# Performance work log

Measured on AMD Instinct MI355X. Metric: run time of the kernel, lower is better.

## Reference

```python
import jax, jax.numpy as jnp
import numpy as np

N = 12288
IN_DIM = 128
OUT_DIM = 128
LR_SLOPE = 0.01
NEG_INF = -9e16


def setup_inputs() -> dict:
    key = jax.random.key(0)
    k1, k2, k3, k4 = jax.random.split(key, 4)
    emb_mat = jax.random.normal(k1, (N, IN_DIM), dtype=jnp.float32)
    adj_mat = jax.random.randint(k2, (N, N), 0, 2, dtype=jnp.int32)
    # xavier-normal-ish init for params
    W = jax.random.normal(k3, (OUT_DIM, IN_DIM), dtype=jnp.float32) * (2.0 / (IN_DIM + OUT_DIM)) ** 0.5
    a = jax.random.normal(k4, (2 * OUT_DIM, 1), dtype=jnp.float32) * (2.0 / (2 * OUT_DIM + 1)) ** 0.5
    return {"emb_mat": emb_mat, "adj_mat": adj_mat, "W": W, "a": a}


def reference(emb_mat, adj_mat, W, a):
    out_dim = W.shape[0]
    e_new = emb_mat @ W.T                       # [N, D_out]
    a1 = a[:out_dim, :]                         # [D_out, 1]
    a2 = a[out_dim:, :]                         # [D_out, 1]
    source_scores = e_new @ a1                  # [N, 1]
    target_scores = e_new @ a2                  # [N, 1]
    e = source_scores + target_scores.T         # [N, N] outer sum
    e = jax.nn.leaky_relu(e, negative_slope=LR_SLOPE)
    e = jnp.where(adj_mat > 0, e, NEG_INF)
    attention = jax.nn.softmax(e, axis=-1)      # [N, N]
    e_transf = attention @ e_new                # [N, D_out]
    return jax.nn.relu(e_transf)
```

## Files before the change

kernel.cpp:

```cpp
#include <hip/hip_runtime.h>


#define NN 12288
#define DIM 128
#define CSPLIT 4
#define COLS_PER (NN / CSPLIT)

typedef __bf16 bf16x8 __attribute__((ext_vector_type(8)));
typedef float f32x4 __attribute__((ext_vector_type(4)));

__global__ __launch_bounds__(256) void k1_gemm(const float* __restrict__ emb,
                                               const float* __restrict__ W,
                                               const float* __restrict__ a,
                                               __bf16* __restrict__ Vt,
                                               float* __restrict__ s,
                                               float* __restrict__ t) {
  const int lane = threadIdx.x & 63;
  const int wave = threadIdx.x >> 6;
  const int m = lane & 15;
  const int quad = lane >> 4;
  const int row0 = blockIdx.x * 128 + wave * 32;

  f32x4 acc[2][8];
#pragma unroll
  for (int mt = 0; mt < 2; mt++)
#pragma unroll
    for (int nb = 0; nb < 8; nb++) acc[mt][nb] = (f32x4){0.f, 0.f, 0.f, 0.f};

#pragma unroll
  for (int ks = 0; ks < 4; ks++) {
    const int k0 = ks * 32 + quad * 8;
    bf16x8 af[2];
#pragma unroll
    for (int mt = 0; mt < 2; mt++) {
      const float* ep = emb + (size_t)(row0 + mt * 16 + m) * DIM + k0;
      float4 lo = *(const float4*)ep;
      float4 hi = *(const float4*)(ep + 4);
      af[mt] = (bf16x8){(__bf16)lo.x, (__bf16)lo.y, (__bf16)lo.z, (__bf16)lo.w,
                        (__bf16)hi.x, (__bf16)hi.y, (__bf16)hi.z, (__bf16)hi.w};
    }
#pragma unroll
    for (int nb = 0; nb < 8; nb++) {
      const float* wp = W + (size_t)(nb * 16 + m) * DIM + k0;
      float4 lo = *(const float4*)wp;
      float4 hi = *(const float4*)(wp + 4);
      bf16x8 bf = {(__bf16)lo.x, (__bf16)lo.y, (__bf16)lo.z, (__bf16)lo.w,
                   (__bf16)hi.x, (__bf16)hi.y, (__bf16)hi.z, (__bf16)hi.w};
      acc[0][nb] = __builtin_amdgcn_mfma_f32_16x16x32_bf16(af[0], bf, acc[0][nb], 0, 0, 0);
      acc[1][nb] = __builtin_amdgcn_mfma_f32_16x16x32_bf16(af[1], bf, acc[1][nb], 0, 0, 0);
    }
  }

  float a1v[8], a2v[8];
#pragma unroll
  for (int nb = 0; nb < 8; nb++) {
    a1v[nb] = a[nb * 16 + m];
    a2v[nb] = a[DIM + nb * 16 + m];
  }
#pragma unroll
  for (int mt = 0; mt < 2; mt++) {
#pragma unroll
    for (int r = 0; r < 4; r++) {
      const int gr = row0 + mt * 16 + quad * 4 + r;
      float ps = 0.f, pt = 0.f;
#pragma unroll
      for (int nb = 0; nb < 8; nb++) {
        float e = acc[mt][nb][r];
        ps += e * a1v[nb];
        pt += e * a2v[nb];
        Vt[(size_t)(nb * 16 + m) * NN + gr] = (__bf16)e;
      }
      ps += __shfl_xor(ps, 1); ps += __shfl_xor(ps, 2);
      ps += __shfl_xor(ps, 4); ps += __shfl_xor(ps, 8);
      pt += __shfl_xor(pt, 1); pt += __shfl_xor(pt, 2);
      pt += __shfl_xor(pt, 4); pt += __shfl_xor(pt, 8);
      if (m == 0) { s[gr] = ps; t[gr] = pt; }
    }
  }
}

__global__ __launch_bounds__(256) void ktmax(const float* __restrict__ t,
                                             float* __restrict__ tmax) {
  __shared__ float red[256];
  float mx = -1e30f;
  for (int i = threadIdx.x; i < NN; i += 256) mx = fmaxf(mx, t[i]);
  red[threadIdx.x] = mx;
  __syncthreads();
  for (int off = 128; off; off >>= 1) {
    if ((int)threadIdx.x < off) red[threadIdx.x] = fmaxf(red[threadIdx.x], red[threadIdx.x + off]);
    __syncthreads();
  }
  if (threadIdx.x == 0) *tmax = red[0];
}

__global__ __launch_bounds__(256) void k2_attn(const int* __restrict__ adj,
                                               const __bf16* __restrict__ Vt,
                                               const float* __restrict__ s,
                                               const float* __restrict__ t,
                                               const float* __restrict__ tmaxp,
                                               float* __restrict__ out,
                                               float* __restrict__ lws) {
  const int lane = threadIdx.x & 63;
  const int wave = threadIdx.x >> 6;
  const int m = lane & 15;
  const int quad = lane >> 4;
  const int row0 = blockIdx.x * 128 + wave * 32;
  const int col0 = blockIdx.y * COLS_PER;
  const int rowA = row0 + m;
  const int rowB = rowA + 16;

  const float Tmax = *tmaxp;
  const float sA = s[rowA], sB = s[rowB];
  const float uA = sA + Tmax, uB = sB + Tmax;
  const float mA = fmaxf(uA, 0.01f * uA);
  const float mB = fmaxf(uB, 0.01f * uB);

  const int* adjA = adj + (size_t)rowA * NN + col0 + quad * 8;
  const int* adjB = adj + (size_t)rowB * NN + col0 + quad * 8;
  const float* tp = t + col0 + quad * 8;
  const __bf16* vp = Vt + (size_t)m * NN + col0 + quad * 8;

  f32x4 accA[8], accB[8];
#pragma unroll
  for (int nb = 0; nb < 8; nb++) {
    accA[nb] = (f32x4){0.f, 0.f, 0.f, 0.f};
    accB[nb] = (f32x4){0.f, 0.f, 0.f, 0.f};
  }
  float lA = 0.f, lB = 0.f;

  for (int kb = 0; kb < COLS_PER; kb += 32) {
    int4 aA0 = *(const int4*)(adjA + kb);
    int4 aA1 = *(const int4*)(adjA + kb + 4);
    int4 aB0 = *(const int4*)(adjB + kb);
    int4 aB1 = *(const int4*)(adjB + kb + 4);
    float4 t0 = *(const float4*)(tp + kb);
    float4 t1 = *(const float4*)(tp + kb + 4);
    bf16x8 bv[8];
#pragma unroll
    for (int nb = 0; nb < 8; nb++)
      bv[nb] = *(const bf16x8*)(vp + (size_t)nb * 16 * NN + kb);

    bf16x8 pA, pB;
#define PEL(frag, jj, tv, av, ss, mm, ll)                               \
    {                                                                   \
      float v = (ss) + (tv);                                            \
      float lv = fmaxf(v, 0.01f * v);                                   \
      float e = ((av) != 0) ? __expf(lv - (mm)) : 0.f;                  \
      (ll) += e;                                                        \
      frag[jj] = (__bf16)e;                                             \
    }
    PEL(pA, 0, t0.x, aA0.x, sA, mA, lA)
    PEL(pA, 1, t0.y, aA0.y, sA, mA, lA)
    PEL(pA, 2, t0.z, aA0.z, sA, mA, lA)
    PEL(pA, 3, t0.w, aA0.w, sA, mA, lA)
    PEL(pA, 4, t1.x, aA1.x, sA, mA, lA)
    PEL(pA, 5, t1.y, aA1.y, sA, mA, lA)
    PEL(pA, 6, t1.z, aA1.z, sA, mA, lA)
    PEL(pA, 7, t1.w, aA1.w, sA, mA, lA)
    PEL(pB, 0, t0.x, aB0.x, sB, mB, lB)
    PEL(pB, 1, t0.y, aB0.y, sB, mB, lB)
    PEL(pB, 2, t0.z, aB0.z, sB, mB, lB)
    PEL(pB, 3, t0.w, aB0.w, sB, mB, lB)
    PEL(pB, 4, t1.x, aB1.x, sB, mB, lB)
    PEL(pB, 5, t1.y, aB1.y, sB, mB, lB)
    PEL(pB, 6, t1.z, aB1.z, sB, mB, lB)
    PEL(pB, 7, t1.w, aB1.w, sB, mB, lB)
#undef PEL

#pragma unroll
    for (int nb = 0; nb < 8; nb++) {
      accA[nb] = __builtin_amdgcn_mfma_f32_16x16x32_bf16(pA, bv[nb], accA[nb], 0, 0, 0);
      accB[nb] = __builtin_amdgcn_mfma_f32_16x16x32_bf16(pB, bv[nb], accB[nb], 0, 0, 0);
    }
  }

  lA += __shfl_xor(lA, 16); lA += __shfl_xor(lA, 32);
  lB += __shfl_xor(lB, 16); lB += __shfl_xor(lB, 32);
  if (quad == 0) {
    atomicAdd(&lws[rowA], lA);
    atomicAdd(&lws[rowB], lB);
  }

#pragma unroll
  for (int nb = 0; nb < 8; nb++) {
#pragma unroll
    for (int r = 0; r < 4; r++) {
      atomicAdd(out + (size_t)(row0 + quad * 4 + r) * DIM + nb * 16 + m, accA[nb][r]);
      atomicAdd(out + (size_t)(row0 + 16 + quad * 4 + r) * DIM + nb * 16 + m, accB[nb][r]);
    }
  }
}

__global__ __launch_bounds__(256) void k3_fin(float* __restrict__ out,
                                              const float* __restrict__ lws) {
  int idx = blockIdx.x * 256 + threadIdx.x;
  float l = lws[idx >> 7];
  float v = out[idx] / l;
  out[idx] = v > 0.f ? v : 0.f;
}

extern "C" void kernel_launch(void* const* d_in, const int* in_sizes, int n_in,
                              void* d_out, int out_size, void* d_ws, size_t ws_size,
                              hipStream_t stream) {
  (void)in_sizes; (void)n_in; (void)out_size; (void)ws_size;
  const float* emb = (const float*)d_in[0];
  const int* adj = (const int*)d_in[1];
  const float* W = (const float*)d_in[2];
  const float* a = (const float*)d_in[3];
  float* out = (float*)d_out;

  char* ws = (char*)d_ws;
  __bf16* Vt = (__bf16*)ws;
  float* s = (float*)(ws + 3145728);
  float* t = (float*)(ws + 3145728 + 49152);
  float* lws = (float*)(ws + 3145728 + 2 * 49152);
  float* tmax = (float*)(ws + 3145728 + 3 * 49152);

  hipMemsetAsync(out, 0, (size_t)NN * DIM * 4, stream);
  hipMemsetAsync(lws, 0, (size_t)NN * 4, stream);

  k1_gemm<<<NN / 128, 256, 0, stream>>>(emb, W, a, Vt, s, t);
  ktmax<<<1, 256, 0, stream>>>(t, tmax);
  dim3 g2(NN / 128, CSPLIT);
  k2_attn<<<g2, 256, 0, stream>>>(adj, Vt, s, t, tmax, out, lws);
  k3_fin<<<NN * DIM / 256, 256, 0, stream>>>(out, lws);
}
```

Measured before the change: 1.008 ms.

## Split attention columns 16 ways with partial buffers and prefetch adjacency loads

Raises the column split of the attention kernel from 4 to 16 so far more blocks are in flight while streaming the adjacency matrix. Per-split output and row-sum partials are now written to workspace and reduced by two new kernels, replacing the float atomics and the memsets. The next iteration's adjacency and t values are loaded into registers ahead of use, and an occupancy hint is added. The first GEMM is retiled to 64 rows per block. The cost is extra workspace traffic for the partial buffers and their reduction.

```diff
diff --git a/kernel.cpp b/kernel.cpp
--- a/kernel.cpp
+++ b/kernel.cpp
@@ -3,7 +3,7 @@
 
 #define NN 12288
 #define DIM 128
-#define CSPLIT 4
+#define CSPLIT 16
 #define COLS_PER (NN / CSPLIT)
 
 typedef __bf16 bf16x8 __attribute__((ext_vector_type(8)));
@@ -19,35 +19,28 @@
   const int wave = threadIdx.x >> 6;
   const int m = lane & 15;
   const int quad = lane >> 4;
-  const int row0 = blockIdx.x * 128 + wave * 32;
-
-  f32x4 acc[2][8];
-#pragma unroll
-  for (int mt = 0; mt < 2; mt++)
-#pragma unroll
-    for (int nb = 0; nb < 8; nb++) acc[mt][nb] = (f32x4){0.f, 0.f, 0.f, 0.f};
+  const int row0 = blockIdx.x * 64 + wave * 16;
+
+  f32x4 acc[8];
+#pragma unroll
+  for (int nb = 0; nb < 8; nb++) acc[nb] = (f32x4){0.f, 0.f, 0.f, 0.f};
 
 #pragma unroll
   for (int ks = 0; ks < 4; ks++) {
     const int k0 = ks * 32 + quad * 8;
-    bf16x8 af[2];
-#pragma unroll
-    for (int mt = 0; mt < 2; mt++) {
-      const float* ep = emb + (size_t)(row0 + mt * 16 + m) * DIM + k0;
-      float4 lo = *(const float4*)ep;
-      float4 hi = *(const float4*)(ep + 4);
-      af[mt] = (bf16x8){(__bf16)lo.x, (__bf16)lo.y, (__bf16)lo.z, (__bf16)lo.w,
-                        (__bf16)hi.x, (__bf16)hi.y, (__bf16)hi.z, (__bf16)hi.w};
-    }
+    const float* ep = emb + (size_t)(row0 + m) * DIM + k0;
+    float4 lo = *(const float4*)ep;
+    float4 hi = *(const float4*)(ep + 4);
+    bf16x8 af = {(__bf16)lo.x, (__bf16)lo.y, (__bf16)lo.z, (__bf16)lo.w,
+                 (__bf16)hi.x, (__bf16)hi.y, (__bf16)hi.z, (__bf16)hi.w};
 #pragma unroll
     for (int nb = 0; nb < 8; nb++) {
       const float* wp = W + (size_t)(nb * 16 + m) * DIM + k0;
-      float4 lo = *(const float4*)wp;
-      float4 hi = *(const float4*)(wp + 4);
-      bf16x8 bf = {(__bf16)lo.x, (__bf16)lo.y, (__bf16)lo.z, (__bf16)lo.w,
-                   (__bf16)hi.x, (__bf16)hi.y, (__bf16)hi.z, (__bf16)hi.w};
-      acc[0][nb] = __builtin_amdgcn_mfma_f32_16x16x32_bf16(af[0], bf, acc[0][nb], 0, 0, 0);
-      acc[1][nb] = __builtin_amdgcn_mfma_f32_16x16x32_bf16(af[1], bf, acc[1][nb], 0, 0, 0);
+      float4 wlo = *(const float4*)wp;
+      float4 whi = *(const float4*)(wp + 4);
+      bf16x8 bf = {(__bf16)wlo.x, (__bf16)wlo.y, (__bf16)wlo.z, (__bf16)wlo.w,
+                   (__bf16)whi.x, (__bf16)whi.y, (__bf16)whi.z, (__bf16)whi.w};
+      acc[nb] = __builtin_amdgcn_mfma_f32_16x16x32_bf16(af, bf, acc[nb], 0, 0, 0);
     }
   }
 
@@ -58,24 +51,21 @@
     a2v[nb] = a[DIM + nb * 16 + m];
   }
 #pragma unroll
-  for (int mt = 0; mt < 2; mt++) {
-#pragma unroll
-    for (int r = 0; r < 4; r++) {
-      const int gr = row0 + mt * 16 + quad * 4 + r;
-      float ps = 0.f, pt = 0.f;
-#pragma unroll
-      for (int nb = 0; nb < 8; nb++) {
-        float e = acc[mt][nb][r];
-        ps += e * a1v[nb];
-        pt += e * a2v[nb];
-        Vt[(size_t)(nb * 16 + m) * NN + gr] = (__bf16)e;
-      }
-      ps += __shfl_xor(ps, 1); ps += __shfl_xor(ps, 2);
-      ps += __shfl_xor(ps, 4); ps += __shfl_xor(ps, 8);
-      pt += __shfl_xor(pt, 1); pt += __shfl_xor(pt, 2);
-      pt += __shfl_xor(pt, 4); pt += __shfl_xor(pt, 8);
-      if (m == 0) { s[gr] = ps; t[gr] = pt; }
-    }
+  for (int r = 0; r < 4; r++) {
+    const int gr = row0 + quad * 4 + r;
+    float ps = 0.f, pt = 0.f;
+#pragma unroll
+    for (int nb = 0; nb < 8; nb++) {
+      float e = acc[nb][r];
+      ps += e * a1v[nb];
+      pt += e * a2v[nb];
+      Vt[(size_t)(nb * 16 + m) * NN + gr] = (__bf16)e;
+    }
+    ps += __shfl_xor(ps, 1); ps += __shfl_xor(ps, 2);
+    ps += __shfl_xor(ps, 4); ps += __shfl_xor(ps, 8);
+    pt += __shfl_xor(pt, 1); pt += __shfl_xor(pt, 2);
+    pt += __shfl_xor(pt, 4); pt += __shfl_xor(pt, 8);
+    if (m == 0) { s[gr] = ps; t[gr] = pt; }
   }
 }
 
@@ -93,19 +83,20 @@
   if (threadIdx.x == 0) *tmax = red[0];
 }
 
-__global__ __launch_bounds__(256) void k2_attn(const int* __restrict__ adj,
-                                               const __bf16* __restrict__ Vt,
-                                               const float* __restrict__ s,
-                                               const float* __restrict__ t,
-                                               const float* __restrict__ tmaxp,
-                                               float* __restrict__ out,
-                                               float* __restrict__ lws) {
+__global__ __launch_bounds__(256, 3) void k2_attn(const int* __restrict__ adj,
+                                                  const __bf16* __restrict__ Vt,
+                                                  const float* __restrict__ s,
+                                                  const float* __restrict__ t,
+                                                  const float* __restrict__ tmaxp,
+                                                  float* __restrict__ part,
+                                                  float* __restrict__ lpart) {
   const int lane = threadIdx.x & 63;
   const int wave = threadIdx.x >> 6;
   const int m = lane & 15;
   const int quad = lane >> 4;
   const int row0 = blockIdx.x * 128 + wave * 32;
-  const int col0 = blockIdx.y * COLS_PER;
+  const int cs = blockIdx.y;
+  const int col0 = cs * COLS_PER;
   const int rowA = row0 + m;
   const int rowB = rowA + 16;
 
@@ -128,13 +119,24 @@
   }
   float lA = 0.f, lB = 0.f;
 
-  for (int kb = 0; kb < COLS_PER; kb += 32) {
-    int4 aA0 = *(const int4*)(adjA + kb);
-    int4 aA1 = *(const int4*)(adjA + kb + 4);
-    int4 aB0 = *(const int4*)(adjB + kb);
-    int4 aB1 = *(const int4*)(adjB + kb + 4);
-    float4 t0 = *(const float4*)(tp + kb);
-    float4 t1 = *(const float4*)(tp + kb + 4);
+  const int iters = COLS_PER / 32;
+  int4 cA0 = *(const int4*)(adjA);
+  int4 cA1 = *(const int4*)(adjA + 4);
+  int4 cB0 = *(const int4*)(adjB);
+  int4 cB1 = *(const int4*)(adjB + 4);
+  float4 ct0 = *(const float4*)(tp);
+  float4 ct1 = *(const float4*)(tp + 4);
+
+  for (int it = 0; it < iters; ++it) {
+    const int kb = it * 32;
+    const int nkb = (it + 1 < iters) ? kb + 32 : kb;
+    int4 nA0 = *(const int4*)(adjA + nkb);
+    int4 nA1 = *(const int4*)(adjA + nkb + 4);
+    int4 nB0 = *(const int4*)(adjB + nkb);
+    int4 nB1 = *(const int4*)(adjB + nkb + 4);
+    float4 nt0 = *(const float4*)(tp + nkb);
+    float4 nt1 = *(const float4*)(tp + nkb + 4);
+
     bf16x8 bv[8];
 #pragma unroll
     for (int nb = 0; nb < 8; nb++)
@@ -149,22 +151,22 @@
       (ll) += e;                                                        \
       frag[jj] = (__bf16)e;                                             \
     }
-    PEL(pA, 0, t0.x, aA0.x, sA, mA, lA)
-    PEL(pA, 1, t0.y, aA0.y, sA, mA, lA)
-    PEL(pA, 2, t0.z, aA0.z, sA, mA, lA)
-    PEL(pA, 3, t0.w, aA0.w, sA, mA, lA)
-    PEL(pA, 4, t1.x, aA1.x, sA, mA, lA)
-    PEL(pA, 5, t1.y, aA1.y, sA, mA, lA)
-    PEL(pA, 6, t1.z, aA1.z, sA, mA, lA)
-    PEL(pA, 7, t1.w, aA1.w, sA, mA, lA)
-    PEL(pB, 0, t0.x, aB0.x, sB, mB, lB)
-    PEL(pB, 1, t0.y, aB0.y, sB, mB, lB)
-    PEL(pB, 2, t0.z, aB0.z, sB, mB, lB)
-    PEL(pB, 3, t0.w, aB0.w, sB, mB, lB)
-    PEL(pB, 4, t1.x, aB1.x, sB, mB, lB)
-    PEL(pB, 5, t1.y, aB1.y, sB, mB, lB)
-    PEL(pB, 6, t1.z, aB1.z, sB, mB, lB)
-    PEL(pB, 7, t1.w, aB1.w, sB, mB, lB)
+    PEL(pA, 0, ct0.x, cA0.x, sA, mA, lA)
+    PEL(pA, 1, ct0.y, cA0.y, sA, mA, lA)
+    PEL(pA, 2, ct0.z, cA0.z, sA, mA, lA)
+    PEL(pA, 3, ct0.w, cA0.w, sA, mA, lA)
+    PEL(pA, 4, ct1.x, cA1.x, sA, mA, lA)
+    PEL(pA, 5, ct1.y, cA1.y, sA, mA, lA)
+    PEL(pA, 6, ct1.z, cA1.z, sA, mA, lA)
+    PEL(pA, 7, ct1.w, cA1.w, sA, mA, lA)
+    PEL(pB, 0, ct0.x, cB0.x, sB, mB, lB)
+    PEL(pB, 1, ct0.y, cB0.y, sB, mB, lB)
+    PEL(pB, 2, ct0.z, cB0.z, sB, mB, lB)
+    PEL(pB, 3, ct0.w, cB0.w, sB, mB, lB)
+    PEL(pB, 4, ct1.x, cB1.x, sB, mB, lB)
+    PEL(pB, 5, ct1.y, cB1.y, sB, mB, lB)
+    PEL(pB, 6, ct1.z, cB1.z, sB, mB, lB)
+    PEL(pB, 7, ct1.w, cB1.w, sB, mB, lB)
 #undef PEL
 
 #pragma unroll
@@ -172,31 +174,57 @@
       accA[nb] = __builtin_amdgcn_mfma_f32_16x16x32_bf16(pA, bv[nb], accA[nb], 0, 0, 0);
       accB[nb] = __builtin_amdgcn_mfma_f32_16x16x32_bf16(pB, bv[nb], accB[nb], 0, 0, 0);
     }
+
+    cA0 = nA0; cA1 = nA1; cB0 = nB0; cB1 = nB1;
+    ct0 = nt0; ct1 = nt1;
   }
 
   lA += __shfl_xor(lA, 16); lA += __shfl_xor(lA, 32);
   lB += __shfl_xor(lB, 16); lB += __shfl_xor(lB, 32);
   if (quad == 0) {
-    atomicAdd(&lws[rowA], lA);
-    atomicAdd(&lws[rowB], lB);
-  }
-
+    lpart[(size_t)cs * NN + rowA] = lA;
+    lpart[(size_t)cs * NN + rowB] = lB;
+  }
+
+  float* po = part + ((size_t)cs * NN + row0) * DIM;
 #pragma unroll
   for (int nb = 0; nb < 8; nb++) {
 #pragma unroll
     for (int r = 0; r < 4; r++) {
-      atomicAdd(out + (size_t)(row0 + quad * 4 + r) * DIM + nb * 16 + m, accA[nb][r]);
-      atomicAdd(out + (size_t)(row0 + 16 + quad * 4 + r) * DIM + nb * 16 + m, accB[nb][r]);
-    }
-  }
-}
-
-__global__ __launch_bounds__(256) void k3_fin(float* __restrict__ out,
-                                              const float* __restrict__ lws) {
-  int idx = blockIdx.x * 256 + threadIdx.x;
-  float l = lws[idx >> 7];
-  float v = out[idx] / l;
-  out[idx] = v > 0.f ? v : 0.f;
+      po[(size_t)(quad * 4 + r) * DIM + nb * 16 + m] = accA[nb][r];
+      po[(size_t)(16 + quad * 4 + r) * DIM + nb * 16 + m] = accB[nb][r];
+    }
+  }
+}
+
+__global__ __launch_bounds__(256) void kl(const float* __restrict__ lpart,
+                                          float* __restrict__ linv) {
+  const int r = blockIdx.x * 256 + threadIdx.x;
+  float l = 0.f;
+#pragma unroll
+  for (int cs = 0; cs < CSPLIT; cs++) l += lpart[(size_t)cs * NN + r];
+  linv[r] = 1.0f / l;
+}
+
+__global__ __launch_bounds__(256) void k3_fin(const float* __restrict__ part,
+                                              const float* __restrict__ linv,
+                                              float* __restrict__ out) {
+  const int idx = blockIdx.x * 256 + threadIdx.x;
+  const int row = idx >> 5;
+  const float4* p4 = (const float4*)part;
+  float4 acc = p4[idx];
+#pragma unroll
+  for (int cs = 1; cs < CSPLIT; cs++) {
+    float4 v = p4[(size_t)cs * (NN * DIM / 4) + idx];
+    acc.x += v.x; acc.y += v.y; acc.z += v.z; acc.w += v.w;
+  }
+  const float li = linv[row];
+  float4 o;
+  o.x = fmaxf(acc.x * li, 0.f);
+  o.y = fmaxf(acc.y * li, 0.f);
+  o.z = fmaxf(acc.z * li, 0.f);
+  o.w = fmaxf(acc.w * li, 0.f);
+  ((float4*)out)[idx] = o;
 }
 
 extern "C" void kernel_launch(void* const* d_in, const int* in_sizes, int n_in,
@@ -212,16 +240,16 @@
   char* ws = (char*)d_ws;
   __bf16* Vt = (__bf16*)ws;
   float* s = (float*)(ws + 3145728);
-  float* t = (float*)(ws + 3145728 + 49152);
-  float* lws = (float*)(ws + 3145728 + 2 * 49152);
-  float* tmax = (float*)(ws + 3145728 + 3 * 49152);
-
-  hipMemsetAsync(out, 0, (size_t)NN * DIM * 4, stream);
-  hipMemsetAsync(lws, 0, (size_t)NN * 4, stream);
-
-  k1_gemm<<<NN / 128, 256, 0, stream>>>(emb, W, a, Vt, s, t);
+  float* t = (float*)(ws + 3194880);
+  float* lpart = (float*)(ws + 3244032);
+  float* linv = (float*)(ws + 4030464);
+  float* tmax = (float*)(ws + 4079616);
+  float* part = (float*)(ws + 4079872);
+
+  k1_gemm<<<NN / 64, 256, 0, stream>>>(emb, W, a, Vt, s, t);
   ktmax<<<1, 256, 0, stream>>>(t, tmax);
   dim3 g2(NN / 128, CSPLIT);
-  k2_attn<<<g2, 256, 0, stream>>>(adj, Vt, s, t, tmax, out, lws);
-  k3_fin<<<NN * DIM / 256, 256, 0, stream>>>(out, lws);
-}
+  k2_attn<<<g2, 256, 0, stream>>>(adj, Vt, s, t, tmax, part, lpart);
+  kl<<<NN / 256, 256, 0, stream>>>(lpart, linv);
+  k3_fin<<<NN * DIM / 4 / 256, 256, 0, stream>>>(part, linv, out);
+}
```

Result: no change. 1.011 ms (+0.2%).
